# Optimization experiments

Measured on AMD Instinct MI355X. Metric: run time of the kernel, lower is better.

The kernel has to match this reference:

```python
import jax, jax.numpy as jnp
import numpy as np

N_NODES = 100_000
E_OFF = 1_500_000
LATENT = 64
MP_STEPS = 3


def setup_inputs() -> dict:
    key = jax.random.key(0)
    ks = jax.random.split(key, 12)
    # lower-triangular graph: all self-loops + random off-diagonal edges with row >= col
    r = jax.random.randint(ks[0], (E_OFF,), 0, N_NODES)
    c = jax.random.randint(ks[1], (E_OFF,), 0, N_NODES)
    diag = jnp.arange(N_NODES)
    edge_row = jnp.concatenate([jnp.maximum(r, c), diag]).astype(jnp.int64)
    edge_col = jnp.concatenate([jnp.minimum(r, c), diag]).astype(jnp.int64)
    E = E_OFF + N_NODES
    # positive weights (gcn_norm takes deg^{-1/2} of weighted degree)
    edge_attr = jax.random.uniform(ks[2], (E,), jnp.float32) + 0.05
    x = jax.random.normal(ks[3], (N_NODES, 1), jnp.float32)
    L = LATENT
    def lin(k, fi, fo):
        return jax.random.normal(k, (fi, fo), jnp.float32) / np.sqrt(fi)
    return {
        "x": x,
        "edge_attr": edge_attr,
        "w_enc": lin(ks[4], 1, L), "b_enc": jnp.zeros((L,), jnp.float32),
        "conv1_w": jax.random.normal(ks[5], (MP_STEPS, L, L), jnp.float32) / np.sqrt(L),
        "conv1_b": jnp.zeros((MP_STEPS, L), jnp.float32),
        "conv2_w": jax.random.normal(ks[6], (MP_STEPS, L, L), jnp.float32) / np.sqrt(L),
        "conv2_b": jnp.zeros((MP_STEPS, L), jnp.float32),
        "dec_w1": lin(ks[7], 2 * L, L), "dec_b1": jnp.zeros((L,), jnp.float32),
        "dec_w2": lin(ks[8], L, 1), "dec_b2": jnp.zeros((1,), jnp.float32),
        "edge_row": edge_row,
        "edge_col": edge_col,
    }


def reference(x, edge_attr, w_enc, b_enc, conv1_w, conv1_b, conv2_w, conv2_b,
              dec_w1, dec_b1, dec_w2, dec_b2, edge_row, edge_col):
    N = x.shape[0]
    # GCN normalization (graph already contains all self-loops, so PyG's
    # add_remaining_self_loops is a no-op and keeps existing loop weights)
    deg = jax.ops.segment_sum(edge_attr, edge_col, num_segments=N)
    dinv = jnp.where(deg > 0, jax.lax.rsqrt(jnp.maximum(deg, 1e-30)), 0.0)
    norm = dinv[edge_row] * edge_attr * dinv[edge_col]  # [E]
    cnt = jnp.maximum(
        jax.ops.segment_sum(jnp.ones_like(edge_attr), edge_col, num_segments=N), 1.0
    )[:, None]  # mean aggregation denominator

    def gcn(h, W, b):
        m = (h @ W)[edge_row] * norm[:, None]           # [E, F] messages
        agg = jax.ops.segment_sum(m, edge_col, num_segments=N) / cnt
        return agg + b

    # node encoder: single Linear (no activation)
    h = x @ w_enc + b_enc
    for i in range(MP_STEPS):
        h = jax.nn.relu(gcn(h, conv1_w[i], conv1_b[i]))
        h = jax.nn.relu(gcn(h, conv2_w[i], conv2_b[i]))

    # edge decoder: gather endpoints, MLP [2L -> L -> 1]
    e = jnp.concatenate([h[edge_row], h[edge_col]], axis=1)
    e = jax.nn.relu(e @ dec_w1 + dec_b1)
    e = (e @ dec_w2 + dec_b2)[:, 0]                      # [E]
    vals = jnp.where(edge_row == edge_col, jax.nn.softplus(e), e)
    return vals
```

## Files before the change

### kernel.cpp

```cpp
#include <hip/hip_runtime.h>
#include <hip/hip_fp16.h>
#include <math.h>

#define L 64
#define FIXS 65536.0f
#define WAITCNT_LGKM0 0xC07F

typedef _Float16 f16x8 __attribute__((ext_vector_type(8)));
typedef float f32x4 __attribute__((ext_vector_type(4)));

#define FMAMIX_LO(acc, pkh, ws) \
    asm("v_fma_mix_f32 %0, %1, %2, %0 op_sel:[0,0,0] op_sel_hi:[1,0,0]" \
        : "+v"(acc) : "v"(pkh), "v"(ws))
#define FMAMIX_HI(acc, pkh, ws) \
    asm("v_fma_mix_f32 %0, %1, %2, %0 op_sel:[1,0,0] op_sel_hi:[1,0,0]" \
        : "+v"(acc) : "v"(pkh), "v"(ws))
#define PKADDRELU(d, a, b) \
    asm("v_pk_add_f16 %0, %1, %2\n\tv_pk_max_f16 %0, %0, 0" \
        : "=v"(d) : "v"(a), "v"(b))

#define GLOAD(xw_, qv_, J) \
    xw_ = (unsigned)__shfl((int)mwv, (J) * 8 + grp); \
    qv_ = h4[(size_t)(xw_ & 0x1FFFFu) * 8 + sub];
#define FMA8(A, qv_, xw_) { \
    float wv_ = __half2float(__ushort_as_half((unsigned short)((xw_) >> 17))); \
    FMAMIX_LO(A[0], (qv_).x, wv_); FMAMIX_HI(A[1], (qv_).x, wv_); \
    FMAMIX_LO(A[2], (qv_).y, wv_); FMAMIX_HI(A[3], (qv_).y, wv_); \
    FMAMIX_LO(A[4], (qv_).z, wv_); FMAMIX_HI(A[5], (qv_).z, wv_); \
    FMAMIX_LO(A[6], (qv_).w, wv_); FMAMIX_HI(A[7], (qv_).w, wv_); }


__global__ void k_hist(const int* __restrict__ col, const float* __restrict__ attr,
                       unsigned* __restrict__ degcnt,
                       int* __restrict__ rank, int E) {
    int e = blockIdx.x * blockDim.x + threadIdx.x;
    if (e < E) {
        int c = col[e];
        unsigned fx = (unsigned)(int)rintf(attr[e] * FIXS);
        unsigned old = atomicAdd(&degcnt[c], (1u << 24) | fx);
        rank[e] = (int)(old >> 24);
    }
}

__global__ void k_dinv(const unsigned* __restrict__ degcnt,
                       float* __restrict__ dinv, int* __restrict__ cntI,
                       float* __restrict__ rcnt, int N) {
    int n = blockIdx.x * blockDim.x + threadIdx.x;
    if (n < N) {
        unsigned p = degcnt[n];
        unsigned cnt = p >> 24;
        float d = (float)(p & 0xFFFFFFu) * (1.0f / FIXS);
        dinv[n] = (d > 0.f) ? (1.0f / sqrtf(fmaxf(d, 1e-30f))) : 0.f;
        cntI[n] = (int)cnt;
        unsigned c = cnt ? cnt : 1u;
        rcnt[n] = 1.0f / (float)c;
    }
}


__global__ __launch_bounds__(256) void k_scan_a(const int* __restrict__ cntI,
                                                int* __restrict__ blockSums, int N) {
    __shared__ int red[4];
    int b = blockIdx.x, t = threadIdx.x;
    int base = b * 1024 + t * 4;
    int s = 0;
    #pragma unroll
    for (int i = 0; i < 4; ++i) { int idx = base + i; if (idx < N) s += cntI[idx]; }
    #pragma unroll
    for (int off = 32; off > 0; off >>= 1) s += __shfl_down(s, off);
    if ((t & 63) == 0) red[t >> 6] = s;
    __syncthreads();
    if (t == 0) blockSums[b] = red[0] + red[1] + red[2] + red[3];
}

__global__ __launch_bounds__(1024) void k_scan_b(int* __restrict__ blockSums, int B,
                                                 int* __restrict__ ptr, int N) {
    __shared__ int sh[1024];
    int t = threadIdx.x;
    sh[t] = (t < B) ? blockSums[t] : 0;
    __syncthreads();
    for (int off = 1; off < 1024; off <<= 1) {
        int v = (t >= off) ? sh[t - off] : 0;
        __syncthreads();
        sh[t] += v;
        __syncthreads();
    }
    if (t < B) blockSums[t] = (t == 0) ? 0 : sh[t - 1];
    if (t == B - 1) ptr[N] = sh[t];
}

__global__ __launch_bounds__(256) void k_scan_c(const int* __restrict__ cntI,
                                                const int* __restrict__ blockSums,
                                                int* __restrict__ ptr, int N) {
    __shared__ int th[256];
    int b = blockIdx.x, t = threadIdx.x;
    int base = b * 1024 + t * 4;
    int v[4]; int s = 0;
    #pragma unroll
    for (int i = 0; i < 4; ++i) {
        int idx = base + i;
        v[i] = (idx < N) ? cntI[idx] : 0;
        s += v[i];
    }
    th[t] = s;
    __syncthreads();
    for (int off = 1; off < 256; off <<= 1) {
        int xv = (t >= off) ? th[t - off] : 0;
        __syncthreads();
        th[t] += xv;
        __syncthreads();
    }
    int pre = ((t == 0) ? 0 : th[t - 1]) + blockSums[b];
    #pragma unroll
    for (int i = 0; i < 4; ++i) {
        int idx = base + i;
        if (idx < N) ptr[idx] = pre;
        pre += v[i];
    }
}


__global__ void k_scatter(const int* __restrict__ row, const int* __restrict__ col,
                          const float* __restrict__ attr, const float* __restrict__ dinv,
                          const int* __restrict__ colptr,
                          int* __restrict__ rank,
                          unsigned* __restrict__ csrX, int E) {
    int e = blockIdx.x * blockDim.x + threadIdx.x;
    if (e < E) {
        int r = row[e], c = col[e];
        int pos = colptr[c] + rank[e];
        float nrm = dinv[r] * attr[e] * dinv[c];
        unsigned short nb = __half_as_ushort(__float2half(nrm));
        csrX[pos] = (unsigned)r | ((unsigned)nb << 17);
        rank[e] = pos;
    }
}


__global__ __launch_bounds__(256) void k_fill(const int* __restrict__ colptr,
                                              int* __restrict__ colof, int N) {
    int lane = threadIdx.x & 63;
    int wid  = (blockIdx.x * blockDim.x + threadIdx.x) >> 6;
    int nw   = (gridDim.x * blockDim.x) >> 6;
    for (int n = wid; n < N; n += nw) {
        int beg = colptr[n], end = colptr[n + 1];
        for (int p = beg + lane; p < end; p += 64) colof[p] = n;
    }
}


__global__ void k_fold(const float* __restrict__ w_enc, const float* __restrict__ b_enc,
                       const float* __restrict__ W1,
                       float* __restrict__ we1, float* __restrict__ be1) {
    int j = threadIdx.x;
    if (j < L) {
        float a = 0.f, b = 0.f;
        for (int f = 0; f < L; ++f) {
            float wv = W1[f * L + j];
            a += w_enc[f] * wv;
            b += b_enc[f] * wv;
        }
        we1[j] = a; be1[j] = b;
    }
}

__global__ void k_encode(const float* __restrict__ x, const float* __restrict__ we1,
                         const float* __restrict__ be1, __half* __restrict__ g, int N) {
    int idx = blockIdx.x * blockDim.x + threadIdx.x;
    if (idx < N * L) {
        int n = idx >> 6, f = idx & 63;
        g[idx] = __float2half(x[n] * we1[f] + be1[f]);
    }
}


__global__ __launch_bounds__(256, 8) void k_agg(const uint4* __restrict__ h4,
        __half* __restrict__ h_out, const float* __restrict__ bias,
        const int* __restrict__ colptr, const unsigned* __restrict__ csrX,
        const float* __restrict__ rcnt, int N) {
    int lane = threadIdx.x & 63;
    int grp  = lane >> 3;
    int sub  = lane & 7;
    int wid  = (blockIdx.x * blockDim.x + threadIdx.x) >> 6;
    int nw   = (gridDim.x * blockDim.x) >> 6;

    float bl8[8];
    #pragma unroll
    for (int i = 0; i < 8; ++i) bl8[i] = bias[8 * sub + i];

    int beg = 0, end = 0; unsigned mw = 0;
    if (wid < N) {
        beg = colptr[wid];
        end = colptr[wid + 1];
        if (beg + lane < end) mw = csrX[beg + lane];
    }

    for (int n = wid; n < N; n += nw) {
        int n2 = n + nw;
        int beg2 = 0, end2 = 0;
        if (n2 < N) { beg2 = colptr[n2]; end2 = colptr[n2 + 1]; }
        float rcv = rcnt[n];

        float va[8];
        #pragma unroll
        for (int i = 0; i < 8; ++i) va[i] = 0.f;

        auto PROC = [&](unsigned mwv, int mm) {
            int kmax = (mm + 7) >> 3;
            int k = 0;
            while (k < kmax) {
                int rem = kmax - k;
                if (rem >= 4) {
                    unsigned x0, x1, x2, x3; uint4 q0, q1, q2, q3;
                    GLOAD(x0, q0, k) GLOAD(x1, q1, k + 1)
                    GLOAD(x2, q2, k + 2) GLOAD(x3, q3, k + 3)
                    FMA8(va, q0, x0) FMA8(va, q1, x1)
                    FMA8(va, q2, x2) FMA8(va, q3, x3)
                    k += 4;
                } else if (rem == 3) {
                    unsigned x0, x1, x2; uint4 q0, q1, q2;
                    GLOAD(x0, q0, k) GLOAD(x1, q1, k + 1) GLOAD(x2, q2, k + 2)
                    FMA8(va, q0, x0) FMA8(va, q1, x1) FMA8(va, q2, x2)
                    k += 3;
                } else if (rem == 2) {
                    unsigned x0, x1; uint4 q0, q1;
                    GLOAD(x0, q0, k) GLOAD(x1, q1, k + 1)
                    FMA8(va, q0, x0) FMA8(va, q1, x1)
                    k += 2;
                } else {
                    unsigned x0; uint4 q0;
                    GLOAD(x0, q0, k)
                    FMA8(va, q0, x0)
                    k += 1;
                }
            }
        };

        int m = end - beg; if (m > 64) m = 64;
        PROC(mw, m);
        for (int base = beg + 64; base < end; base += 64) {
            int mm = end - base; if (mm > 64) mm = 64;
            unsigned mwc = 0;
            if (lane < mm) mwc = csrX[base + lane];
            PROC(mwc, mm);
        }

        unsigned mw2 = 0;
        if (n2 < N && beg2 + lane < end2) mw2 = csrX[beg2 + lane];

        float s[8];
        #pragma unroll
        for (int i = 0; i < 8; ++i) {
            float v = va[i];
            v += __shfl_xor(v, 8);
            v += __shfl_xor(v, 16);
            v += __shfl_xor(v, 32);
            s[i] = v;
        }
        if (lane < 8) {
            unsigned u[4];
            #pragma unroll
            for (int i = 0; i < 4; ++i) {
                float oa = fmaxf(s[2 * i]     * rcv + bl8[2 * i],     0.f);
                float ob = fmaxf(s[2 * i + 1] * rcv + bl8[2 * i + 1], 0.f);
                u[i] = (unsigned)__half_as_ushort(__float2half(oa))
                     | ((unsigned)__half_as_ushort(__float2half(ob)) << 16);
            }
            uint4 st; st.x = u[0]; st.y = u[1]; st.z = u[2]; st.w = u[3];
            ((uint4*)h_out)[(size_t)n * 8 + lane] = st;
        }

        beg = beg2; end = end2; mw = mw2;
    }
}


__global__ __launch_bounds__(256) void k_gx(const __half* __restrict__ h,
        const float* __restrict__ W, __half* __restrict__ g, int N) {
    int lane = threadIdx.x & 63;
    int wid  = (blockIdx.x * blockDim.x + threadIdx.x) >> 6;
    int nw   = (gridDim.x * blockDim.x) >> 6;
    int r16  = lane & 15;
    int q4   = lane >> 4;

    f16x8 bh[4][2], bl[4][2];
    #pragma unroll
    for (int t = 0; t < 4; ++t)
        #pragma unroll
        for (int ks = 0; ks < 2; ++ks)
            #pragma unroll
            for (int i = 0; i < 8; ++i) {
                int k = ks * 32 + q4 * 8 + i;
                float wv = W[k * L + t * 16 + r16];
                _Float16 hi = (_Float16)wv;
                bh[t][ks][i] = hi;
                bl[t][ks][i] = (_Float16)(wv - (float)hi);
            }

    int tiles = (N + 15) >> 4;
    for (int tt = wid; tt < tiles; tt += nw) {
        int n0 = tt << 4;
        int row = n0 + r16; if (row >= N) row = N - 1;
        f16x8 a0 = *(const f16x8*)(h + (size_t)row * L + q4 * 8);
        f16x8 a1 = *(const f16x8*)(h + (size_t)row * L + 32 + q4 * 8);
        #pragma unroll
        for (int t = 0; t < 4; ++t) {
            f32x4 acc = {0.f, 0.f, 0.f, 0.f};
            acc = __builtin_amdgcn_mfma_f32_16x16x32_f16(a0, bl[t][0], acc, 0, 0, 0);
            acc = __builtin_amdgcn_mfma_f32_16x16x32_f16(a1, bl[t][1], acc, 0, 0, 0);
            acc = __builtin_amdgcn_mfma_f32_16x16x32_f16(a0, bh[t][0], acc, 0, 0, 0);
            acc = __builtin_amdgcn_mfma_f32_16x16x32_f16(a1, bh[t][1], acc, 0, 0, 0);
            #pragma unroll
            for (int r = 0; r < 4; ++r) {
                int node = n0 + q4 * 4 + r;
                if (node < N)
                    g[(size_t)node * L + t * 16 + r16] = __float2half(acc[r]);
            }
        }
    }
}


__global__ __launch_bounds__(256) void k_mv2(const __half* __restrict__ h,
        const float* __restrict__ W1, const float* __restrict__ b1,
        __half* __restrict__ U, __half* __restrict__ V, int N) {
    int lane = threadIdx.x & 63;
    int wid  = (blockIdx.x * blockDim.x + threadIdx.x) >> 6;
    int nw   = (gridDim.x * blockDim.x) >> 6;
    int r16  = lane & 15;
    int q4   = lane >> 4;
    int tiles = (N + 15) >> 4;

    for (int phase = 0; phase < 2; ++phase) {
        const float* W = W1 + (size_t)phase * L * L;
        __half* O = phase ? V : U;
        f16x8 bh[4][2], bl[4][2];
        float bv[4];
        #pragma unroll
        for (int t = 0; t < 4; ++t) {
            bv[t] = phase ? 0.f : b1[t * 16 + r16];
            #pragma unroll
            for (int ks = 0; ks < 2; ++ks)
                #pragma unroll
                for (int i = 0; i < 8; ++i) {
                    int k = ks * 32 + q4 * 8 + i;
                    float wv = W[k * L + t * 16 + r16];
                    _Float16 hi = (_Float16)wv;
                    bh[t][ks][i] = hi;
                    bl[t][ks][i] = (_Float16)(wv - (float)hi);
                }
        }
        for (int tt = wid; tt < tiles; tt += nw) {
            int n0 = tt << 4;
            int row = n0 + r16; if (row >= N) row = N - 1;
            f16x8 a0 = *(const f16x8*)(h + (size_t)row * L + q4 * 8);
            f16x8 a1 = *(const f16x8*)(h + (size_t)row * L + 32 + q4 * 8);
            #pragma unroll
            for (int t = 0; t < 4; ++t) {
                f32x4 acc = {0.f, 0.f, 0.f, 0.f};
                acc = __builtin_amdgcn_mfma_f32_16x16x32_f16(a0, bl[t][0], acc, 0, 0, 0);
                acc = __builtin_amdgcn_mfma_f32_16x16x32_f16(a1, bl[t][1], acc, 0, 0, 0);
                acc = __builtin_amdgcn_mfma_f32_16x16x32_f16(a0, bh[t][0], acc, 0, 0, 0);
                acc = __builtin_amdgcn_mfma_f32_16x16x32_f16(a1, bh[t][1], acc, 0, 0, 0);
                #pragma unroll
                for (int r = 0; r < 4; ++r) {
                    int node = n0 + q4 * 4 + r;
                    if (node < N)
                        O[(size_t)node * L + t * 16 + r16] = __float2half(acc[r] + bv[t]);
                }
            }
        }
    }
}


__global__ __launch_bounds__(256, 8) void k_edge(const __half* __restrict__ U,
        const __half* __restrict__ V, const float* __restrict__ w2,
        const float* __restrict__ b2, const unsigned* __restrict__ csrX,
        const int* __restrict__ colof, float* __restrict__ tmp, int E) {
    int sub = threadIdx.x & 7;
    float w2f[8];
    #pragma unroll
    for (int i = 0; i < 8; ++i) w2f[i] = w2[8 * sub + i];
    float b2v = b2[0];
    int tid = blockIdx.x * blockDim.x + threadIdx.x;
    int np  = (gridDim.x * blockDim.x) >> 3;
    for (int p = tid >> 3; p < E; p += np) {
        unsigned md = csrX[p];
        int r = (int)(md & 0x1FFFFu);
        int n = colof[p];
        uint4 uq = ((const uint4*)(U + (size_t)r * L))[sub];
        uint4 vq = ((const uint4*)(V + (size_t)n * L))[sub];
        float p0 = 0.f, p1 = 0.f;
        #define DOT2X(uw_, vw_, B) { unsigned t_; \
            PKADDRELU(t_, (uw_), (vw_)); \
            FMAMIX_LO(p0, t_, w2f[B]); FMAMIX_HI(p1, t_, w2f[(B) + 1]); }
        DOT2X(uq.x, vq.x, 0) DOT2X(uq.y, vq.y, 2)
        DOT2X(uq.z, vq.z, 4) DOT2X(uq.w, vq.w, 6)
        #undef DOT2X
        float pd = p0 + p1;
        pd += __shfl_xor(pd, 1);
        pd += __shfl_xor(pd, 2);
        pd += __shfl_xor(pd, 4);
        if (sub == 0) tmp[p] = pd + b2v;
    }
}


__global__ void k_perm(const int* __restrict__ epos, const float* __restrict__ tmp,
                       const int* __restrict__ erow, const int* __restrict__ ecol,
                       float* __restrict__ out, int E) {
    int e = blockIdx.x * blockDim.x + threadIdx.x;
    if (e < E) {
        float val = tmp[epos[e]];
        if (erow[e] == ecol[e])
            val = fmaxf(val, 0.f) + log1pf(expf(-fabsf(val)));
        out[e] = val;
    }
}


extern "C" void kernel_launch(void* const* d_in, const int* in_sizes, int n_in,
                              void* d_out, int out_size, void* d_ws, size_t ws_size,
                              hipStream_t stream) {
    const float* x     = (const float*)d_in[0];
    const float* attr  = (const float*)d_in[1];
    const float* w_enc = (const float*)d_in[2];
    const float* b_enc = (const float*)d_in[3];
    const float* c1w   = (const float*)d_in[4];
    const float* c1b   = (const float*)d_in[5];
    const float* c2w   = (const float*)d_in[6];
    const float* c2b   = (const float*)d_in[7];
    const float* dw1   = (const float*)d_in[8];
    const float* db1   = (const float*)d_in[9];
    const float* dw2   = (const float*)d_in[10];
    const float* db2   = (const float*)d_in[11];
    const int*   erow  = (const int*)d_in[12];
    const int*   ecol  = (const int*)d_in[13];
    int N = in_sizes[0];
    int E = in_sizes[1];
    float* out = (float*)d_out;

    char* w = (char*)d_ws;
    auto alloc = [&](size_t bytes) {
        char* p = w; w += (bytes + 255) & ~(size_t)255; return p;
    };
    unsigned* degcnt = (unsigned*)alloc((size_t)N * 4);
    size_t zbytes = (size_t)(w - (char*)d_ws);
    float* dinv   = (float*)alloc((size_t)N * 4);
    int*   cntI   = (int*)  alloc((size_t)N * 4);
    float* rcnt   = (float*)alloc((size_t)N * 4);
    int*   colptr = (int*)  alloc((size_t)(N + 1) * 4);
    int*   bsums  = (int*)  alloc(((size_t)(N + 1023) / 1024 + 1) * 4);
    float* we1    = (float*)alloc(L * 4);
    float* be1    = (float*)alloc(L * 4);
    int*   rank   = (int*)  alloc((size_t)E * 4);
    unsigned* csrX = (unsigned*)alloc((size_t)E * 4);
    int*   colof  = (int*)  alloc((size_t)E * 4);
    float* tmp    = (float*)alloc((size_t)E * 4);
    __half* hA    = (__half*)alloc((size_t)N * L * 2);
    __half* hB    = (__half*)alloc((size_t)N * L * 2);
    __half* hU    = (__half*)alloc((size_t)N * L * 2);
    __half* hV    = (__half*)alloc((size_t)N * L * 2);
    __half* gbuf  = hU;
    (void)ws_size; (void)n_in; (void)out_size;

    (void)hipMemsetAsync(d_ws, 0, zbytes, stream);

    int eb = (E + 255) / 256;
    int nb = (N + 255) / 256;
    int B  = (N + 1023) / 1024;
    k_hist<<<eb, 256, 0, stream>>>(ecol, attr, degcnt, rank, E);
    k_dinv<<<nb, 256, 0, stream>>>(degcnt, dinv, cntI, rcnt, N);
    k_scan_a<<<B, 256, 0, stream>>>(cntI, bsums, N);
    k_scan_b<<<1, 1024, 0, stream>>>(bsums, B, colptr, N);
    k_scan_c<<<B, 256, 0, stream>>>(cntI, bsums, colptr, N);
    k_scatter<<<eb, 256, 0, stream>>>(erow, ecol, attr, dinv, colptr, rank, csrX, E);
    k_fill<<<1024, 256, 0, stream>>>(colptr, colof, N);

    k_fold<<<1, 64, 0, stream>>>(w_enc, b_enc, c1w, we1, be1);
    k_encode<<<(N * L + 255) / 256, 256, 0, stream>>>(x, we1, be1, gbuf, N);

    const float* Ws[6] = {c1w,             c2w,
                          c1w + L * L,     c2w + L * L,
                          c1w + 2 * L * L, c2w + 2 * L * L};
    const float* Bs[6] = {c1b,         c2b,
                          c1b + L,     c2b + L,
                          c1b + 2 * L, c2b + 2 * L};
    (void)Ws[0];
    __half* outs[2] = {hA, hB};
    __half* hcur = nullptr;
    for (int j = 0; j < 6; ++j) {
        hcur = outs[j & 1];
        k_agg<<<2048, 256, 0, stream>>>((const uint4*)gbuf, hcur, Bs[j],
                                        colptr, csrX, rcnt, N);
        if (j < 5)
            k_gx<<<512, 256, 0, stream>>>(hcur, Ws[j + 1], gbuf, N);
    }
    k_mv2<<<512, 256, 0, stream>>>(hcur, dw1, db1, hU, hV, N);
    k_edge<<<2048, 256, 0, stream>>>(hU, hV, dw2, db2, csrX, colof, tmp, E);
    k_perm<<<eb, 256, 0, stream>>>(rank, tmp, erow, ecol, out, E);
}
```

Measured before the change: 564.0 us.

## Software-pipeline neighbor feature gathers one node ahead in aggregation kernel

The aggregation kernel now keeps two nodes of CSR metadata in flight and, for nodes with at most 32 in-edges, issues the gathered feature loads for the next node before processing the current one. Each wave overlaps the memory latency of the next node's gathers with the current node's FMA and reduction work. Nodes with more edges fall back to the original loop. The extra uint4 registers lower the occupancy hint from 8 to 5 blocks per CU, which trades wave-level parallelism for per-wave memory-level parallelism.

```diff
diff --git a/kernel.cpp b/kernel.cpp
--- a/kernel.cpp
+++ b/kernel.cpp
@@ -174,7 +174,7 @@
 }
 
 
-__global__ __launch_bounds__(256, 8) void k_agg(const uint4* __restrict__ h4,
+__global__ __launch_bounds__(256, 5) void k_agg(const uint4* __restrict__ h4,
         __half* __restrict__ h_out, const float* __restrict__ bias,
         const int* __restrict__ colptr, const unsigned* __restrict__ csrX,
         const float* __restrict__ rcnt, int N) {
@@ -188,65 +188,110 @@
     #pragma unroll
     for (int i = 0; i < 8; ++i) bl8[i] = bias[8 * sub + i];
 
-    int beg = 0, end = 0; unsigned mw = 0;
+    int beg0 = 0, end0 = 0; unsigned mw0 = 0;
+    int beg1 = 0, end1 = 0; unsigned mw1 = 0;
     if (wid < N) {
-        beg = colptr[wid];
-        end = colptr[wid + 1];
-        if (beg + lane < end) mw = csrX[beg + lane];
+        beg0 = colptr[wid]; end0 = colptr[wid + 1];
+        if (beg0 + lane < end0) mw0 = csrX[beg0 + lane];
+    }
+    if (wid + nw < N) {
+        beg1 = colptr[wid + nw]; end1 = colptr[wid + nw + 1];
+        if (beg1 + lane < end1) mw1 = csrX[beg1 + lane];
+    }
+
+    uint4 sq0, sq1, sq2, sq3;
+    unsigned sx0 = 0, sx1 = 0, sx2 = 0, sx3 = 0;
+    int curSk = -1;
+    {
+        int m0 = end0 - beg0;
+        if (wid < N && m0 <= 32) {
+            curSk = (m0 + 7) >> 3;
+            if (curSk > 0) { sx0 = (unsigned)__shfl((int)mw0, grp);
+                             sq0 = h4[(size_t)(sx0 & 0x1FFFFu) * 8 + sub]; }
+            if (curSk > 1) { sx1 = (unsigned)__shfl((int)mw0, 8 + grp);
+                             sq1 = h4[(size_t)(sx1 & 0x1FFFFu) * 8 + sub]; }
+            if (curSk > 2) { sx2 = (unsigned)__shfl((int)mw0, 16 + grp);
+                             sq2 = h4[(size_t)(sx2 & 0x1FFFFu) * 8 + sub]; }
+            if (curSk > 3) { sx3 = (unsigned)__shfl((int)mw0, 24 + grp);
+                             sq3 = h4[(size_t)(sx3 & 0x1FFFFu) * 8 + sub]; }
+        }
     }
 
     for (int n = wid; n < N; n += nw) {
-        int n2 = n + nw;
-        int beg2 = 0, end2 = 0;
-        if (n2 < N) { beg2 = colptr[n2]; end2 = colptr[n2 + 1]; }
         float rcv = rcnt[n];
+
+        int nSk = -1;
+        unsigned nx0 = 0, nx1 = 0, nx2 = 0, nx3 = 0;
+        uint4 nq0, nq1, nq2, nq3;
+        int m1 = end1 - beg1;
+        if (n + nw < N && m1 <= 32) {
+            nSk = (m1 + 7) >> 3;
+            if (nSk > 0) { nx0 = (unsigned)__shfl((int)mw1, grp);
+                           nq0 = h4[(size_t)(nx0 & 0x1FFFFu) * 8 + sub]; }
+            if (nSk > 1) { nx1 = (unsigned)__shfl((int)mw1, 8 + grp);
+                           nq1 = h4[(size_t)(nx1 & 0x1FFFFu) * 8 + sub]; }
+            if (nSk > 2) { nx2 = (unsigned)__shfl((int)mw1, 16 + grp);
+                           nq2 = h4[(size_t)(nx2 & 0x1FFFFu) * 8 + sub]; }
+            if (nSk > 3) { nx3 = (unsigned)__shfl((int)mw1, 24 + grp);
+                           nq3 = h4[(size_t)(nx3 & 0x1FFFFu) * 8 + sub]; }
+        }
+
+        int begp = beg1, endp = end1; unsigned mwp = mw1;
+        int n2 = n + 2 * nw;
+        if (n2 < N) {
+            beg1 = colptr[n2]; end1 = colptr[n2 + 1];
+            mw1 = (beg1 + lane < end1) ? csrX[beg1 + lane] : 0;
+        } else { beg1 = 0; end1 = 0; mw1 = 0; }
 
         float va[8];
         #pragma unroll
         for (int i = 0; i < 8; ++i) va[i] = 0.f;
 
-        auto PROC = [&](unsigned mwv, int mm) {
-            int kmax = (mm + 7) >> 3;
-            int k = 0;
-            while (k < kmax) {
-                int rem = kmax - k;
-                if (rem >= 4) {
-                    unsigned x0, x1, x2, x3; uint4 q0, q1, q2, q3;
-                    GLOAD(x0, q0, k) GLOAD(x1, q1, k + 1)
-                    GLOAD(x2, q2, k + 2) GLOAD(x3, q3, k + 3)
-                    FMA8(va, q0, x0) FMA8(va, q1, x1)
-                    FMA8(va, q2, x2) FMA8(va, q3, x3)
-                    k += 4;
-                } else if (rem == 3) {
-                    unsigned x0, x1, x2; uint4 q0, q1, q2;
-                    GLOAD(x0, q0, k) GLOAD(x1, q1, k + 1) GLOAD(x2, q2, k + 2)
-                    FMA8(va, q0, x0) FMA8(va, q1, x1) FMA8(va, q2, x2)
-                    k += 3;
-                } else if (rem == 2) {
-                    unsigned x0, x1; uint4 q0, q1;
-                    GLOAD(x0, q0, k) GLOAD(x1, q1, k + 1)
-                    FMA8(va, q0, x0) FMA8(va, q1, x1)
-                    k += 2;
-                } else {
-                    unsigned x0; uint4 q0;
-                    GLOAD(x0, q0, k)
-                    FMA8(va, q0, x0)
-                    k += 1;
+        if (curSk >= 0) {
+            if (curSk > 0) FMA8(va, sq0, sx0)
+            if (curSk > 1) FMA8(va, sq1, sx1)
+            if (curSk > 2) FMA8(va, sq2, sx2)
+            if (curSk > 3) FMA8(va, sq3, sx3)
+        } else {
+            auto PROC = [&](unsigned mwv, int mm) {
+                int kmax = (mm + 7) >> 3;
+                int k = 0;
+                while (k < kmax) {
+                    int rem = kmax - k;
+                    if (rem >= 4) {
+                        unsigned x0, x1, x2, x3; uint4 q0, q1, q2, q3;
+                        GLOAD(x0, q0, k) GLOAD(x1, q1, k + 1)
+                        GLOAD(x2, q2, k + 2) GLOAD(x3, q3, k + 3)
+                        FMA8(va, q0, x0) FMA8(va, q1, x1)
+                        FMA8(va, q2, x2) FMA8(va, q3, x3)
+                        k += 4;
+                    } else if (rem == 3) {
+                        unsigned x0, x1, x2; uint4 q0, q1, q2;
+                        GLOAD(x0, q0, k) GLOAD(x1, q1, k + 1) GLOAD(x2, q2, k + 2)
+                        FMA8(va, q0, x0) FMA8(va, q1, x1) FMA8(va, q2, x2)
+                        k += 3;
+                    } else if (rem == 2) {
+                        unsigned x0, x1; uint4 q0, q1;
+                        GLOAD(x0, q0, k) GLOAD(x1, q1, k + 1)
+                        FMA8(va, q0, x0) FMA8(va, q1, x1)
+                        k += 2;
+                    } else {
+                        unsigned x0; uint4 q0;
+                        GLOAD(x0, q0, k)
+                        FMA8(va, q0, x0)
+                        k += 1;
+                    }
                 }
+            };
+            int m = end0 - beg0; if (m > 64) m = 64;
+            PROC(mw0, m);
+            for (int base = beg0 + 64; base < end0; base += 64) {
+                int mm = end0 - base; if (mm > 64) mm = 64;
+                unsigned mwc = 0;
+                if (lane < mm) mwc = csrX[base + lane];
+                PROC(mwc, mm);
             }
-        };
-
-        int m = end - beg; if (m > 64) m = 64;
-        PROC(mw, m);
-        for (int base = beg + 64; base < end; base += 64) {
-            int mm = end - base; if (mm > 64) mm = 64;
-            unsigned mwc = 0;
-            if (lane < mm) mwc = csrX[base + lane];
-            PROC(mwc, mm);
-        }
-
-        unsigned mw2 = 0;
-        if (n2 < N && beg2 + lane < end2) mw2 = csrX[beg2 + lane];
+        }
 
         float s[8];
         #pragma unroll
@@ -270,7 +315,10 @@
             ((uint4*)h_out)[(size_t)n * 8 + lane] = st;
         }
 
-        beg = beg2; end = end2; mw = mw2;
+        beg0 = begp; end0 = endp; mw0 = mwp;
+        curSk = nSk;
+        sx0 = nx0; sx1 = nx1; sx2 = nx2; sx3 = nx3;
+        sq0 = nq0; sq1 = nq1; sq2 = nq2; sq3 = nq3;
     }
 }
 
```

After: 619.3 us. 9.8% more time.

## Build CSC via two-level LDS counting sort instead of global atomic histogram

Applied to the files above, without the earlier changes.

Replaces the global-atomic degree histogram and rank-based scatter with a two-pass bucketed counting sort. Pass one histograms edges by column>>8 per block in LDS, a scan gives global offsets, edges are scattered as 16-byte payloads, and a per-bucket kernel sorts within 256 columns using LDS atomics while computing counts, degrees and colptr. The aim is to remove contended global atomics and the memset, and to make the final permutation a coalesced read with scattered writes. It adds more kernels and extra payload traffic, and folds softplus for self-loops into the edge kernel.

```diff
diff --git a/kernel.cpp b/kernel.cpp
--- a/kernel.cpp
+++ b/kernel.cpp
@@ -30,30 +30,112 @@
     FMAMIX_LO(A[6], (qv_).w, wv_); FMAMIX_HI(A[7], (qv_).w, wv_); }
 
 
-__global__ void k_hist(const int* __restrict__ col, const float* __restrict__ attr,
-                       unsigned* __restrict__ degcnt,
-                       int* __restrict__ rank, int E) {
-    int e = blockIdx.x * blockDim.x + threadIdx.x;
-    if (e < E) {
-        int c = col[e];
-        unsigned fx = (unsigned)(int)rintf(attr[e] * FIXS);
-        unsigned old = atomicAdd(&degcnt[c], (1u << 24) | fx);
-        rank[e] = (int)(old >> 24);
-    }
-}
-
-__global__ void k_dinv(const unsigned* __restrict__ degcnt,
-                       float* __restrict__ dinv, int* __restrict__ cntI,
-                       float* __restrict__ rcnt, int N) {
+#define EPB 4096
+
+__global__ __launch_bounds__(256) void k_s1(const int* __restrict__ ecol,
+        int* __restrict__ ghist, int NBLK, int DHI, int E) {
+    __shared__ unsigned hist[512];
+    int t = threadIdx.x, blk = blockIdx.x;
+    for (int d = t; d < 512; d += 256) hist[d] = 0;
+    __syncthreads();
+    #pragma unroll
+    for (int it = 0; it < EPB / 256; ++it) {
+        int e = blk * EPB + it * 256 + t;
+        if (e < E) atomicAdd(&hist[(unsigned)ecol[e] >> 8], 1u);
+    }
+    __syncthreads();
+    for (int d = t; d < DHI; d += 256)
+        ghist[(size_t)d * NBLK + blk] = (int)hist[d];
+}
+
+__global__ __launch_bounds__(256) void k_s3(const int* __restrict__ erow,
+        const int* __restrict__ ecol, const float* __restrict__ attr,
+        const int* __restrict__ gq, uint4* __restrict__ pay,
+        int NBLK, int DHI, int E) {
+    __shared__ int bases[512];
+    __shared__ unsigned cnt[512];
+    int t = threadIdx.x, blk = blockIdx.x;
+    for (int d = t; d < DHI; d += 256) {
+        bases[d] = gq[(size_t)d * NBLK + blk];
+        cnt[d] = 0;
+    }
+    __syncthreads();
+    #pragma unroll
+    for (int it = 0; it < EPB / 256; ++it) {
+        int e = blk * EPB + it * 256 + t;
+        if (e < E) {
+            unsigned c = (unsigned)ecol[e];
+            int d = (int)(c >> 8);
+            int lr = (int)atomicAdd(&cnt[d], 1u);
+            int pos = bases[d] + lr;
+            uint4 pl;
+            pl.x = (unsigned)erow[e] | ((c & 255u) << 17);
+            pl.y = (unsigned)e;
+            pl.z = __float_as_uint(attr[e]);
+            pl.w = 0;
+            pay[pos] = pl;
+        }
+    }
+}
+
+__global__ __launch_bounds__(256) void k_s4(const uint4* __restrict__ pay,
+        const int* __restrict__ gq,
+        unsigned* __restrict__ rowS, float* __restrict__ attrS,
+        int* __restrict__ colptr, int* __restrict__ cntI,
+        unsigned* __restrict__ degS, int* __restrict__ inv,
+        int NBLK, int N) {
+    __shared__ unsigned cntA[256], sumA[256], cnt2[256];
+    __shared__ int sh[256], colStart[256];
+    int t = threadIdx.x, hd = blockIdx.x;
+    cntA[t] = 0; sumA[t] = 0; cnt2[t] = 0;
+    __syncthreads();
+    int start = gq[(size_t)hd * NBLK];
+    int end   = gq[(size_t)(hd + 1) * NBLK];
+    for (int i = start + t; i < end; i += 256) {
+        uint4 pl = pay[i];
+        int j = (int)((pl.x >> 17) & 255u);
+        atomicAdd(&cntA[j], 1u);
+        unsigned fx = (unsigned)(int)rintf(__uint_as_float(pl.z) * FIXS);
+        atomicAdd(&sumA[j], fx);
+    }
+    __syncthreads();
+    sh[t] = (int)cntA[t];
+    __syncthreads();
+    for (int off = 1; off < 256; off <<= 1) {
+        int v = (t >= off) ? sh[t - off] : 0;
+        __syncthreads();
+        sh[t] += v;
+        __syncthreads();
+    }
+    colStart[t] = sh[t] - (int)cntA[t];
+    int col = hd * 256 + t;
+    if (col < N) {
+        colptr[col] = start + colStart[t];
+        cntI[col]   = (int)cntA[t];
+        degS[col]   = sumA[t];
+    }
+    __syncthreads();
+    for (int i = start + t; i < end; i += 256) {
+        uint4 pl = pay[i];
+        int j = (int)((pl.x >> 17) & 255u);
+        int lr = (int)atomicAdd(&cnt2[j], 1u);
+        int pos = start + colStart[j] + lr;
+        rowS[pos]  = pl.x;
+        attrS[pos] = __uint_as_float(pl.z);
+        inv[pos]   = (int)pl.y;
+    }
+}
+
+__global__ void k_dinv(const unsigned* __restrict__ degS, const int* __restrict__ cntI,
+                       float* __restrict__ dinv, float* __restrict__ rcnt,
+                       int* __restrict__ colptr, int N, int E) {
     int n = blockIdx.x * blockDim.x + threadIdx.x;
     if (n < N) {
-        unsigned p = degcnt[n];
-        unsigned cnt = p >> 24;
-        float d = (float)(p & 0xFFFFFFu) * (1.0f / FIXS);
+        float d = (float)degS[n] * (1.0f / FIXS);
         dinv[n] = (d > 0.f) ? (1.0f / sqrtf(fmaxf(d, 1e-30f))) : 0.f;
-        cntI[n] = (int)cnt;
-        unsigned c = cnt ? cnt : 1u;
+        int c = cntI[n]; if (c < 1) c = 1;
         rcnt[n] = 1.0f / (float)c;
+        if (n == 0) colptr[N] = E;
     }
 }
 
@@ -116,23 +198,6 @@
         int idx = base + i;
         if (idx < N) ptr[idx] = pre;
         pre += v[i];
-    }
-}
-
-
-__global__ void k_scatter(const int* __restrict__ row, const int* __restrict__ col,
-                          const float* __restrict__ attr, const float* __restrict__ dinv,
-                          const int* __restrict__ colptr,
-                          int* __restrict__ rank,
-                          unsigned* __restrict__ csrX, int E) {
-    int e = blockIdx.x * blockDim.x + threadIdx.x;
-    if (e < E) {
-        int r = row[e], c = col[e];
-        int pos = colptr[c] + rank[e];
-        float nrm = dinv[r] * attr[e] * dinv[c];
-        unsigned short nb = __half_as_ushort(__float2half(nrm));
-        csrX[pos] = (unsigned)r | ((unsigned)nb << 17);
-        rank[e] = pos;
     }
 }
 
@@ -145,6 +210,19 @@
     for (int n = wid; n < N; n += nw) {
         int beg = colptr[n], end = colptr[n + 1];
         for (int p = beg + lane; p < end; p += 64) colof[p] = n;
+    }
+}
+
+
+__global__ void k_norm(const unsigned* __restrict__ rowS, const float* __restrict__ attrS,
+                       const int* __restrict__ colof, const float* __restrict__ dinv,
+                       unsigned* __restrict__ csrX, int E) {
+    int p = blockIdx.x * blockDim.x + threadIdx.x;
+    if (p < E) {
+        unsigned row = rowS[p] & 0x1FFFFu;
+        float nrm = dinv[row] * attrS[p] * dinv[colof[p]];
+        unsigned short nb = __half_as_ushort(__float2half(nrm));
+        csrX[p] = row | ((unsigned)nb << 17);
     }
 }
 
@@ -402,21 +480,19 @@
         pd += __shfl_xor(pd, 1);
         pd += __shfl_xor(pd, 2);
         pd += __shfl_xor(pd, 4);
-        if (sub == 0) tmp[p] = pd + b2v;
-    }
-}
-
-
-__global__ void k_perm(const int* __restrict__ epos, const float* __restrict__ tmp,
-                       const int* __restrict__ erow, const int* __restrict__ ecol,
+        if (sub == 0) {
+            float val = pd + b2v;
+            if (r == n) val = fmaxf(val, 0.f) + log1pf(expf(-fabsf(val)));
+            tmp[p] = val;
+        }
+    }
+}
+
+
+__global__ void k_perm(const int* __restrict__ inv, const float* __restrict__ tmp,
                        float* __restrict__ out, int E) {
-    int e = blockIdx.x * blockDim.x + threadIdx.x;
-    if (e < E) {
-        float val = tmp[epos[e]];
-        if (erow[e] == ecol[e])
-            val = fmaxf(val, 0.f) + log1pf(expf(-fabsf(val)));
-        out[e] = val;
-    }
+    int p = blockIdx.x * blockDim.x + threadIdx.x;
+    if (p < E) out[inv[p]] = tmp[p];
 }
 
 
@@ -441,20 +517,25 @@
     int E = in_sizes[1];
     float* out = (float*)d_out;
 
+    int DHI  = (N + 255) >> 8;
+    int NBLK = (E + EPB - 1) / EPB;
+    int M    = DHI * NBLK;
+
     char* w = (char*)d_ws;
     auto alloc = [&](size_t bytes) {
         char* p = w; w += (bytes + 255) & ~(size_t)255; return p;
     };
-    unsigned* degcnt = (unsigned*)alloc((size_t)N * 4);
-    size_t zbytes = (size_t)(w - (char*)d_ws);
+    unsigned* degS  = (unsigned*)alloc((size_t)N * 4);
+    int*   cntI   = (int*)  alloc((size_t)N * 4);
     float* dinv   = (float*)alloc((size_t)N * 4);
-    int*   cntI   = (int*)  alloc((size_t)N * 4);
     float* rcnt   = (float*)alloc((size_t)N * 4);
     int*   colptr = (int*)  alloc((size_t)(N + 1) * 4);
-    int*   bsums  = (int*)  alloc(((size_t)(N + 1023) / 1024 + 1) * 4);
+    int*   bsums  = (int*)  alloc(1025 * 4);
     float* we1    = (float*)alloc(L * 4);
     float* be1    = (float*)alloc(L * 4);
-    int*   rank   = (int*)  alloc((size_t)E * 4);
+    int*   ghist  = (int*)  alloc((size_t)M * 4);
+    int*   gq     = (int*)  alloc((size_t)(M + 1) * 4);
+    int*   inv    = (int*)  alloc((size_t)E * 4);
     unsigned* csrX = (unsigned*)alloc((size_t)E * 4);
     int*   colof  = (int*)  alloc((size_t)E * 4);
     float* tmp    = (float*)alloc((size_t)E * 4);
@@ -462,21 +543,26 @@
     __half* hB    = (__half*)alloc((size_t)N * L * 2);
     __half* hU    = (__half*)alloc((size_t)N * L * 2);
     __half* hV    = (__half*)alloc((size_t)N * L * 2);
-    __half* gbuf  = hU;
+    uint4*    pay   = (uint4*)hA;
+    unsigned* rowS  = (unsigned*)hU;
+    float*    attrS = (float*)hV;
+    __half*   gbuf  = hU;
     (void)ws_size; (void)n_in; (void)out_size;
-
-    (void)hipMemsetAsync(d_ws, 0, zbytes, stream);
 
     int eb = (E + 255) / 256;
     int nb = (N + 255) / 256;
-    int B  = (N + 1023) / 1024;
-    k_hist<<<eb, 256, 0, stream>>>(ecol, attr, degcnt, rank, E);
-    k_dinv<<<nb, 256, 0, stream>>>(degcnt, dinv, cntI, rcnt, N);
-    k_scan_a<<<B, 256, 0, stream>>>(cntI, bsums, N);
-    k_scan_b<<<1, 1024, 0, stream>>>(bsums, B, colptr, N);
-    k_scan_c<<<B, 256, 0, stream>>>(cntI, bsums, colptr, N);
-    k_scatter<<<eb, 256, 0, stream>>>(erow, ecol, attr, dinv, colptr, rank, csrX, E);
+    int Bm = (M + 1023) / 1024;
+
+    k_s1<<<NBLK, 256, 0, stream>>>(ecol, ghist, NBLK, DHI, E);
+    k_scan_a<<<Bm, 256, 0, stream>>>(ghist, bsums, M);
+    k_scan_b<<<1, 1024, 0, stream>>>(bsums, Bm, gq, M);
+    k_scan_c<<<Bm, 256, 0, stream>>>(ghist, bsums, gq, M);
+    k_s3<<<NBLK, 256, 0, stream>>>(erow, ecol, attr, gq, pay, NBLK, DHI, E);
+    k_s4<<<DHI, 256, 0, stream>>>(pay, gq, rowS, attrS, colptr, cntI, degS, inv,
+                                  NBLK, N);
+    k_dinv<<<nb, 256, 0, stream>>>(degS, cntI, dinv, rcnt, colptr, N, E);
     k_fill<<<1024, 256, 0, stream>>>(colptr, colof, N);
+    k_norm<<<eb, 256, 0, stream>>>(rowS, attrS, colof, dinv, csrX, E);
 
     k_fold<<<1, 64, 0, stream>>>(w_enc, b_enc, c1w, we1, be1);
     k_encode<<<(N * L + 255) / 256, 256, 0, stream>>>(x, we1, be1, gbuf, N);
@@ -499,5 +585,5 @@
     }
     k_mv2<<<512, 256, 0, stream>>>(hcur, dw1, db1, hU, hV, N);
     k_edge<<<2048, 256, 0, stream>>>(hU, hV, dw2, db2, csrX, colof, tmp, E);
-    k_perm<<<eb, 256, 0, stream>>>(rank, tmp, erow, ecol, out, E);
-}
+    k_perm<<<eb, 256, 0, stream>>>(inv, tmp, out, E);
+}
```

Result: slower. 580.5 us (+2.9%).
